# Optimization experiments

Hardware: AMD Instinct MI355X
Metric: run time of the kernel (lower is better)

## Reference

```python
import jax, jax.numpy as jnp
import numpy as np

W_DIM = 512
C_IN = 512
C_OUT = 512
K = 3
EPS = 1e-6
STYLE_SCALE = 1.0 / np.sqrt(W_DIM)              # EqualizedWeight scale for (out,in)
CONV_SCALE = 1.0 / np.sqrt(C_IN * K * K)        # EqualizedWeight scale for (out,in,k,k)


def setup_inputs() -> dict:
    key = jax.random.key(0)
    ks = jax.random.split(key, 6)
    B, H, W = 16, 64, 64
    return {
        "x": jax.random.normal(ks[0], (B, C_IN, H, W), dtype=jnp.float32),
        "w": jax.random.normal(ks[1], (B, W_DIM), dtype=jnp.float32),
        "style_weight": jax.random.normal(ks[2], (C_IN, W_DIM), dtype=jnp.float32),
        "style_bias": jnp.zeros((C_IN,), dtype=jnp.float32),
        "conv_weight": jax.random.normal(ks[3], (C_OUT, C_IN, K, K), dtype=jnp.float32),
        "noise_weight": jax.random.normal(ks[4], (1, C_OUT, 1, 1), dtype=jnp.float32),
        "bias": jnp.zeros((C_OUT,), dtype=jnp.float32),
        "noise": jax.random.normal(ks[5], (B, 1, H, W), dtype=jnp.float32),
    }


def reference(x, w, style_weight, style_bias, conv_weight, noise_weight, bias, noise):
    B, _, H, Wd = x.shape
    # to_style: equalized linear  [B, C_IN]
    s = w @ (style_weight * STYLE_SCALE).T + style_bias
    # modulate: [B, C_OUT, C_IN, K, K]
    wts = (conv_weight * CONV_SCALE)[None] * s[:, None, :, None, None]
    # demodulate
    sigma = jax.lax.rsqrt(jnp.sum(wts * wts, axis=(2, 3, 4)) + EPS)  # [B, C_OUT]
    wts = wts * sigma[:, :, None, None, None]
    # grouped conv with groups = batch
    x_r = x.reshape(1, B * C_IN, H, Wd)
    w_r = wts.reshape(B * C_OUT, C_IN, K, K)
    y = jax.lax.conv_general_dilated(
        x_r, w_r, window_strides=(1, 1), padding=[(1, 1), (1, 1)],
        dimension_numbers=("NCHW", "OIHW", "NCHW"), feature_group_count=B,
    ).reshape(B, C_OUT, H, Wd)
    # noise injection + bias + leaky relu(0.2)
    y = y + noise_weight * noise + bias[None, :, None, None]
    return jax.nn.leaky_relu(y, negative_slope=0.2)
```

## Files before the change

### kernel.cpp

```cpp
#include <hip/hip_runtime.h>


typedef __attribute__((ext_vector_type(8))) short short8;
typedef __attribute__((ext_vector_type(4))) float f32x4;

#define STYLE_SCALE 0.044194173824159216f
#define CONV_SCALE  0.014731391274719742f
#define CS2         (1.0f/4608.0f)

static __device__ __forceinline__ unsigned short f2bf(float x) {
    union { float f; unsigned int u; } a; a.f = x;
    unsigned int r = a.u + 0x7fffu + ((a.u >> 16) & 1u);
    return (unsigned short)(r >> 16);
}

static __device__ __forceinline__ void gl_lds16(const void* g, void* l) {
    __builtin_amdgcn_global_load_lds(
        (const __attribute__((address_space(1))) unsigned int*)g,
        (__attribute__((address_space(3))) unsigned int*)l, 16, 0, 0);
}

__global__ void k_style(const float* __restrict__ w, const float* __restrict__ sw,
                        const float* __restrict__ sb, float* __restrict__ s) {
    int b = blockIdx.y, j0 = blockIdx.x * 64, t = threadIdx.x;
    __shared__ float wl[512];
    __shared__ float part[256];
    wl[t] = w[b*512 + t]; wl[t+256] = w[b*512 + t + 256];
    __syncthreads();
    int jl = t & 63, seg = t >> 6;
    const float4* row = (const float4*)(sw + (size_t)(j0 + jl)*512) + seg*32;
    const float*  wv  = wl + seg*128;
    float acc = 0.f;
#pragma unroll 4
    for (int k = 0; k < 32; ++k) {
        float4 v = row[k];
        acc += v.x*wv[4*k] + v.y*wv[4*k+1] + v.z*wv[4*k+2] + v.w*wv[4*k+3];
    }
    part[t] = acc;
    __syncthreads();
    if (t < 64)
        s[b*512 + j0 + t] = (part[t] + part[t+64] + part[t+128] + part[t+192])
                            * STYLE_SCALE + sb[j0 + t];
}

__global__ void k_wprep(const float* __restrict__ cw, float* __restrict__ csq,
                        unsigned short* __restrict__ cwt) {
    int o = blockIdx.x, t = threadIdx.x;
    __shared__ float row[4608];
    const float4* src = (const float4*)(cw + (size_t)o*4608);
    for (int i = t; i < 1152; i += 256) ((float4*)row)[i] = src[i];
    __syncthreads();
#pragma unroll
    for (int it = 0; it < 2; ++it) {
        int i = t + it*256;
        float a = 0.f;
#pragma unroll
        for (int k = 0; k < 9; ++k) { float v = row[i*9 + k]; a += v*v; }
        csq[(size_t)o*512 + i] = a * CS2;
    }
    for (int p = t; p < 576; p += 256) {
        int ic = p / 36, rem = p % 36;
        int tap = rem >> 2, g = rem & 3;
        int i0 = ic*32 + g*8;
        union { unsigned short us[8]; uint4 q; } u;
#pragma unroll
        for (int j = 0; j < 8; ++j)
            u.us[j] = f2bf(row[(i0 + j)*9 + tap] * CONV_SCALE);
        size_t dst = (((size_t)(o >> 6)*16 + ic)*36 + rem)*64 + (o & 63);
        *(uint4*)(cwt + dst*8) = u.q;
    }
}

__global__ void k_sigma(const float* __restrict__ s, const float* __restrict__ csq,
                        float* __restrict__ sig) {
    int b = blockIdx.y, o0 = blockIdx.x * 64, t = threadIdx.x;
    __shared__ float s2l[512];
    __shared__ float part[256];
    float v0 = s[b*512 + t], v1 = s[b*512 + t + 256];
    s2l[t] = v0*v0; s2l[t+256] = v1*v1;
    __syncthreads();
    int ol = t & 63, seg = t >> 6;
    const float4* row = (const float4*)(csq + (size_t)(o0 + ol)*512) + seg*32;
    const float*  sv  = s2l + seg*128;
    float acc = 0.f;
#pragma unroll 4
    for (int k = 0; k < 32; ++k) {
        float4 c = row[k];
        acc += c.x*sv[4*k] + c.y*sv[4*k+1] + c.z*sv[4*k+2] + c.w*sv[4*k+3];
    }
    part[t] = acc;
    __syncthreads();
    if (t < 64)
        sig[b*512 + o0 + t] = 1.0f / sqrtf(part[t] + part[t+64] + part[t+128]
                                           + part[t+192] + 1e-6f);
}

__global__ void k_xt(const float* __restrict__ x, const float* __restrict__ s,
                     unsigned short* __restrict__ xt) {
    int h = blockIdx.x, b = blockIdx.y, t = threadIdx.x;
    __shared__ float tile[64][65];
    __shared__ float sl[64];
    for (int c0 = 0; c0 < 512; c0 += 64) {
        if (t < 64) sl[t] = s[b*512 + c0 + t];
#pragma unroll
        for (int it = 0; it < 4; ++it) {
            int idx = t + it*256;
            int c = idx >> 4, w4 = (idx & 15) * 4;
            float4 v = *(const float4*)(x + ((size_t)(b*512 + c0 + c)*4096) + h*64 + w4);
            tile[c][w4]   = v.x; tile[c][w4+1] = v.y;
            tile[c][w4+2] = v.z; tile[c][w4+3] = v.w;
        }
        __syncthreads();
#pragma unroll
        for (int it = 0; it < 2; ++it) {
            int idx = t + it*256;
            int wq = idx >> 3, c = (idx & 7) * 8;
            union { unsigned short us[8]; uint4 q; } u;
#pragma unroll
            for (int j = 0; j < 8; ++j)
                u.us[j] = f2bf(tile[c + j][wq] * sl[c + j]);
            *(uint4*)(xt + ((size_t)(b*4096 + h*64 + wq)*512 + c0 + c)) = u.q;
        }
        __syncthreads();
    }
}

__global__ __launch_bounds__(256, 2)
void k_conv(const unsigned short* __restrict__ xt, const unsigned short* __restrict__ cwt,
            const float* __restrict__ sig, const float* __restrict__ nw,
            const float* __restrict__ bias, const float* __restrict__ noise,
            float* __restrict__ out) {
    __shared__ __align__(16) short xs_s[2][20480];

    const int tid  = threadIdx.x;
    const int lane = tid & 63;
    const int wave = tid >> 6;
    const int quad = lane >> 4;
    const int l15  = lane & 15;

    const int flat  = blockIdx.x;
    const int chunk = flat & 7, idx = flat >> 3;
    const int pxblk = idx & 7;
    const int oblk  = (idx >> 3) & 7;
    const int b     = chunk*2 + (idx >> 6);
    const int o0 = oblk * 64, h0 = pxblk * 8;

    if (h0 == 0)
        for (int i = tid; i < 1024; i += 256) {
            ((unsigned int*)xs_s[0])[i] = 0u;
            ((unsigned int*)xs_s[1])[i] = 0u;
        }
    if (h0 == 56)
        for (int i = tid; i < 1024; i += 256) {
            ((unsigned int*)xs_s[0])[9*1024 + i] = 0u;
            ((unsigned int*)xs_s[1])[9*1024 + i] = 0u;
        }

    const int pp = lane >> 2;
    const int cg = (lane & 3) ^ ((lane >> 3) & 3);

#define STAGE(bufidx, icn) do {                                              \
        short* dst_ = xs_s[bufidx];                                          \
        for (int q_ = wave; q_ < 40; q_ += 4) {                              \
            int r_ = q_ >> 2, p0_ = (q_ & 3) << 4;                           \
            int gr_ = h0 - 1 + r_;                                           \
            if (gr_ >= 0 && gr_ < 64)                                        \
                gl_lds16(xt + ((size_t)(b*4096 + gr_*64 + p0_ + pp)*512      \
                               + (icn)*32 + cg*8),                           \
                         dst_ + (r_*64 + p0_)*32);                           \
        } } while (0)

    f32x4 acc[2][4][4];
#pragma unroll
    for (int rr = 0; rr < 2; ++rr)
#pragma unroll
        for (int mt = 0; mt < 4; ++mt)
#pragma unroll
            for (int nt = 0; nt < 4; ++nt) acc[rr][mt][nt] = (f32x4){0.f,0.f,0.f,0.f};

    const unsigned short* cwbase = cwt + (size_t)oblk*294912 + (size_t)quad*512
                                       + (size_t)l15*8;

    STAGE(0, 0);
    __syncthreads();

    for (int ic = 0; ic < 16; ++ic) {
        const unsigned short* cwA = cwbase + (size_t)ic*18432;
        const short8* xp = (const short8*)xs_s[ic & 1];
        const short8 z8 = {};

#define LOADA(dst, tap) do { _Pragma("unroll")                               \
        for (int mt_ = 0; mt_ < 4; ++mt_)                                    \
            dst[mt_] = *(const short8*)(cwA + (tap)*2048 + mt_*128);         \
        } while (0)

        short8 a0A[4], a0B[4];
        LOADA(a0A, 0);
        LOADA(a0B, 3);
        __builtin_amdgcn_sched_barrier(0);
        if (ic < 15) STAGE((ic + 1) & 1, ic + 1);
        __builtin_amdgcn_sched_barrier(0);

#define TAPSTEP(AF, C0, C1) do { _Pragma("unroll")                           \
        for (int mt_ = 0; mt_ < 4; ++mt_) { _Pragma("unroll")                \
            for (int nt_ = 0; nt_ < 4; ++nt_) {                              \
                acc[0][mt_][nt_] = __builtin_amdgcn_mfma_f32_16x16x32_bf16(  \
                    AF[mt_], C0[nt_], acc[0][mt_][nt_], 0, 0, 0);            \
                acc[1][mt_][nt_] = __builtin_amdgcn_mfma_f32_16x16x32_bf16(  \
                    AF[mt_], C1[nt_], acc[1][mt_][nt_], 0, 0, 0);            \
            } } } while (0)

#define LOADB(bf, d, dx, colS) do {                                          \
            const int base_ = (2*wave + (d))*256 + (colS);                   \
            if ((dx) == 0) {                                                 \
                int a0_ = (l15 == 0) ? base_ : base_ - 64;                   \
                bf[0] = xp[a0_];        bf[1] = xp[base_];                   \
                bf[2] = xp[base_ + 64]; bf[3] = xp[base_ + 128];             \
                if (l15 == 0) bf[0] = z8;                                    \
            } else if ((dx) == 1) {                                          \
                bf[0] = xp[base_ - 64]; bf[1] = xp[base_];                   \
                bf[2] = xp[base_ + 64]; bf[3] = xp[base_ + 128];             \
            } else {                                                         \
                int a3_ = (l15 == 15) ? base_ : base_ + 128;                 \
                bf[0] = xp[base_ - 64]; bf[1] = xp[base_];                   \
                bf[2] = xp[base_ + 64]; bf[3] = xp[a3_];                     \
            }                                                                \
        } while (0)

#define DXBODY(dx, AFA, AFB) do {                                            \
            const int cs_   = l15 + (dx) + 15;                               \
            const int slot_ = quad ^ ((cs_ >> 1) & 3);                       \
            const int colS_ = cs_*4 + slot_;                                 \
            short8 bA[4], bB[4];                                             \
            LOADB(bA, 0, dx, colS_);                                         \
            LOADB(bB, 1, dx, colS_);                                         \
            if ((dx) == 2 && l15 == 15) { bA[3] = z8; bB[3] = z8; }          \
            TAPSTEP(AFA, bA, bB);                                            \
            LOADA(AFA, (dx) + 6);          \
            LOADB(bA, 2, dx, colS_);                                         \
            if ((dx) == 2 && l15 == 15) bA[3] = z8;                          \
            TAPSTEP(AFB, bB, bA);                                            \
            LOADB(bB, 3, dx, colS_);                                         \
            if ((dx) == 2 && l15 == 15) bB[3] = z8;                          \
            TAPSTEP(AFA, bA, bB);                                            \
        } while (0)

        DXBODY(0, a0A, a0B);
        {
            short8 a1A[4], a1B[4];
            LOADA(a1A, 1); LOADA(a1B, 4);
            DXBODY(1, a1A, a1B);
        }
        {
            short8 a2A[4], a2B[4];
            LOADA(a2A, 2); LOADA(a2B, 5);
            DXBODY(2, a2A, a2B);
        }
#undef DXBODY
#undef LOADB
#undef TAPSTEP
#undef LOADA
        __syncthreads();
    }
#undef STAGE

    float nz[2][4];
#pragma unroll
    for (int rr = 0; rr < 2; ++rr) {
        int h = h0 + 2*wave + rr;
#pragma unroll
        for (int nt = 0; nt < 4; ++nt) nz[rr][nt] = noise[b*4096 + h*64 + nt*16 + l15];
    }
#pragma unroll
    for (int mt = 0; mt < 4; ++mt) {
#pragma unroll
        for (int r = 0; r < 4; ++r) {
            int o = o0 + mt*16 + quad*4 + r;
            float sg  = sig[b*512 + o];
            float nwv = nw[o], bv = bias[o];
#pragma unroll
            for (int rr = 0; rr < 2; ++rr) {
                int h = h0 + 2*wave + rr;
#pragma unroll
                for (int nt = 0; nt < 4; ++nt) {
                    float v = acc[rr][mt][nt][r] * sg + nwv * nz[rr][nt] + bv;
                    v = (v >= 0.f) ? v : 0.2f * v;
                    out[((size_t)(b*512 + o)*4096) + h*64 + nt*16 + l15] = v;
                }
            }
        }
    }
}

extern "C" void kernel_launch(void* const* d_in, const int* in_sizes, int n_in,
                              void* d_out, int out_size, void* d_ws, size_t ws_size,
                              hipStream_t stream) {
    const float* x     = (const float*)d_in[0];
    const float* w     = (const float*)d_in[1];
    const float* sw    = (const float*)d_in[2];
    const float* sb    = (const float*)d_in[3];
    const float* cw    = (const float*)d_in[4];
    const float* nw    = (const float*)d_in[5];
    const float* bias  = (const float*)d_in[6];
    const float* noise = (const float*)d_in[7];
    float* out = (float*)d_out;

    char* ws = (char*)d_ws;
    unsigned short* xt  = (unsigned short*)(ws + 0);
    unsigned short* cwt = (unsigned short*)(ws + 67108864);
    float* s   = (float*)(ws + 71827456);
    float* sig = (float*)(ws + 71860224);
    float* csq = (float*)(ws + 71892992);

    k_wprep<<<512, 256, 0, stream>>>(cw, csq, cwt);
    k_style<<<dim3(8, 16), 256, 0, stream>>>(w, sw, sb, s);
    k_sigma<<<dim3(8, 16), 256, 0, stream>>>(s, csq, sig);
    k_xt   <<<dim3(64, 16), 256, 0, stream>>>(x, s, xt);
    k_conv <<<dim3(1024), 256, 0, stream>>>(xt, cwt, sig, nw, bias, noise, out);
}
```

Before: 494.7 us.

## Halve conv row tile to raise occupancy, add MFMA setprio

Each conv block now computes 4 output rows instead of 8, so each wave owns one row. This halves the accumulator registers and shrinks the LDS halo buffer, allowing 3 blocks per CU and doubling the grid. MFMA bursts are wrapped in s_setprio and the A-fragment loads are restructured per dx. The cost is more redundant halo loads (6 rows staged per 4 rows computed) and twice as many weight-fragment reloads per output pixel.

```diff
diff --git a/kernel.cpp b/kernel.cpp
--- a/kernel.cpp
+++ b/kernel.cpp
@@ -125,12 +125,12 @@
     }
 }
 
-__global__ __launch_bounds__(256, 2)
+__global__ __launch_bounds__(256, 3)
 void k_conv(const unsigned short* __restrict__ xt, const unsigned short* __restrict__ cwt,
             const float* __restrict__ sig, const float* __restrict__ nw,
             const float* __restrict__ bias, const float* __restrict__ noise,
             float* __restrict__ out) {
-    __shared__ __align__(16) short xs_s[2][20480];
+    __shared__ __align__(16) short xs_s[2][6*64*32];
 
     const int tid  = threadIdx.x;
     const int lane = tid & 63;
@@ -140,20 +140,20 @@
 
     const int flat  = blockIdx.x;
     const int chunk = flat & 7, idx = flat >> 3;
-    const int pxblk = idx & 7;
-    const int oblk  = (idx >> 3) & 7;
-    const int b     = chunk*2 + (idx >> 6);
-    const int o0 = oblk * 64, h0 = pxblk * 8;
+    const int pxblk = idx & 15;
+    const int oblk  = (idx >> 4) & 7;
+    const int b     = chunk*2 + (idx >> 7);
+    const int o0 = oblk * 64, h0 = pxblk * 4;
 
     if (h0 == 0)
         for (int i = tid; i < 1024; i += 256) {
             ((unsigned int*)xs_s[0])[i] = 0u;
             ((unsigned int*)xs_s[1])[i] = 0u;
         }
-    if (h0 == 56)
+    if (h0 == 60)
         for (int i = tid; i < 1024; i += 256) {
-            ((unsigned int*)xs_s[0])[9*1024 + i] = 0u;
-            ((unsigned int*)xs_s[1])[9*1024 + i] = 0u;
+            ((unsigned int*)xs_s[0])[5*1024 + i] = 0u;
+            ((unsigned int*)xs_s[1])[5*1024 + i] = 0u;
         }
 
     const int pp = lane >> 2;
@@ -161,7 +161,7 @@
 
 #define STAGE(bufidx, icn) do {                                              \
         short* dst_ = xs_s[bufidx];                                          \
-        for (int q_ = wave; q_ < 40; q_ += 4) {                              \
+        for (int q_ = wave; q_ < 24; q_ += 4) {                              \
             int r_ = q_ >> 2, p0_ = (q_ & 3) << 4;                           \
             int gr_ = h0 - 1 + r_;                                           \
             if (gr_ >= 0 && gr_ < 64)                                        \
@@ -170,48 +170,43 @@
                          dst_ + (r_*64 + p0_)*32);                           \
         } } while (0)
 
-    f32x4 acc[2][4][4];
-#pragma unroll
-    for (int rr = 0; rr < 2; ++rr)
-#pragma unroll
-        for (int mt = 0; mt < 4; ++mt)
-#pragma unroll
-            for (int nt = 0; nt < 4; ++nt) acc[rr][mt][nt] = (f32x4){0.f,0.f,0.f,0.f};
+    f32x4 acc[4][4];
+#pragma unroll
+    for (int mt = 0; mt < 4; ++mt)
+#pragma unroll
+        for (int nt = 0; nt < 4; ++nt) acc[mt][nt] = (f32x4){0.f,0.f,0.f,0.f};
 
     const unsigned short* cwbase = cwt + (size_t)oblk*294912 + (size_t)quad*512
                                        + (size_t)l15*8;
 
     STAGE(0, 0);
     __syncthreads();
+
+    const short8 z8 = {};
 
     for (int ic = 0; ic < 16; ++ic) {
         const unsigned short* cwA = cwbase + (size_t)ic*18432;
         const short8* xp = (const short8*)xs_s[ic & 1];
-        const short8 z8 = {};
+        if (ic < 15) STAGE((ic + 1) & 1, ic + 1);
 
 #define LOADA(dst, tap) do { _Pragma("unroll")                               \
         for (int mt_ = 0; mt_ < 4; ++mt_)                                    \
             dst[mt_] = *(const short8*)(cwA + (tap)*2048 + mt_*128);         \
         } while (0)
 
-        short8 a0A[4], a0B[4];
-        LOADA(a0A, 0);
-        LOADA(a0B, 3);
-        __builtin_amdgcn_sched_barrier(0);
-        if (ic < 15) STAGE((ic + 1) & 1, ic + 1);
-        __builtin_amdgcn_sched_barrier(0);
-
-#define TAPSTEP(AF, C0, C1) do { _Pragma("unroll")                           \
+#define TAP(AF, BF) do {                                                     \
+        __builtin_amdgcn_s_setprio(1);                                       \
+        _Pragma("unroll")                                                    \
         for (int mt_ = 0; mt_ < 4; ++mt_) { _Pragma("unroll")                \
-            for (int nt_ = 0; nt_ < 4; ++nt_) {                              \
-                acc[0][mt_][nt_] = __builtin_amdgcn_mfma_f32_16x16x32_bf16(  \
-                    AF[mt_], C0[nt_], acc[0][mt_][nt_], 0, 0, 0);            \
-                acc[1][mt_][nt_] = __builtin_amdgcn_mfma_f32_16x16x32_bf16(  \
-                    AF[mt_], C1[nt_], acc[1][mt_][nt_], 0, 0, 0);            \
-            } } } while (0)
+            for (int nt_ = 0; nt_ < 4; ++nt_)                                \
+                acc[mt_][nt_] = __builtin_amdgcn_mfma_f32_16x16x32_bf16(     \
+                    AF[mt_], BF[nt_], acc[mt_][nt_], 0, 0, 0);               \
+        }                                                                    \
+        __builtin_amdgcn_s_setprio(0);                                       \
+        } while (0)
 
 #define LOADB(bf, d, dx, colS) do {                                          \
-            const int base_ = (2*wave + (d))*256 + (colS);                   \
+            const int base_ = (wave + (d))*256 + (colS);                     \
             if ((dx) == 0) {                                                 \
                 int a0_ = (l15 == 0) ? base_ : base_ - 64;                   \
                 bf[0] = xp[a0_];        bf[1] = xp[base_];                   \
@@ -227,50 +222,39 @@
             }                                                                \
         } while (0)
 
-#define DXBODY(dx, AFA, AFB) do {                                            \
+#define DXBODY(dx) do {                                                      \
             const int cs_   = l15 + (dx) + 15;                               \
             const int slot_ = quad ^ ((cs_ >> 1) & 3);                       \
             const int colS_ = cs_*4 + slot_;                                 \
-            short8 bA[4], bB[4];                                             \
-            LOADB(bA, 0, dx, colS_);                                         \
-            LOADB(bB, 1, dx, colS_);                                         \
-            if ((dx) == 2 && l15 == 15) { bA[3] = z8; bB[3] = z8; }          \
-            TAPSTEP(AFA, bA, bB);                                            \
-            LOADA(AFA, (dx) + 6);          \
-            LOADB(bA, 2, dx, colS_);                                         \
-            if ((dx) == 2 && l15 == 15) bA[3] = z8;                          \
-            TAPSTEP(AFB, bB, bA);                                            \
-            LOADB(bB, 3, dx, colS_);                                         \
-            if ((dx) == 2 && l15 == 15) bB[3] = z8;                          \
-            TAPSTEP(AFA, bA, bB);                                            \
+            short8 af[4], ag[4], b0[4], b1[4];                               \
+            LOADA(af, dx);                                 \
+            LOADA(ag, (dx) + 3);                           \
+            LOADB(b0, 0, dx, colS_);                                         \
+            LOADB(b1, 1, dx, colS_);                                         \
+            if ((dx) == 2 && l15 == 15) { b0[3] = z8; b1[3] = z8; }          \
+            TAP(af, b0);                                                     \
+            LOADA(af, (dx) + 6);                 \
+            LOADB(b0, 2, dx, colS_);            \
+            if ((dx) == 2 && l15 == 15) b0[3] = z8;                          \
+            TAP(ag, b1);                                                     \
+            TAP(af, b0);                                                     \
         } while (0)
 
-        DXBODY(0, a0A, a0B);
-        {
-            short8 a1A[4], a1B[4];
-            LOADA(a1A, 1); LOADA(a1B, 4);
-            DXBODY(1, a1A, a1B);
-        }
-        {
-            short8 a2A[4], a2B[4];
-            LOADA(a2A, 2); LOADA(a2B, 5);
-            DXBODY(2, a2A, a2B);
-        }
+        DXBODY(0);
+        DXBODY(1);
+        DXBODY(2);
 #undef DXBODY
 #undef LOADB
-#undef TAPSTEP
+#undef TAP
 #undef LOADA
         __syncthreads();
     }
 #undef STAGE
 
-    float nz[2][4];
-#pragma unroll
-    for (int rr = 0; rr < 2; ++rr) {
-        int h = h0 + 2*wave + rr;
-#pragma unroll
-        for (int nt = 0; nt < 4; ++nt) nz[rr][nt] = noise[b*4096 + h*64 + nt*16 + l15];
-    }
+    const int h = h0 + wave;
+    float nz[4];
+#pragma unroll
+    for (int nt = 0; nt < 4; ++nt) nz[nt] = noise[b*4096 + h*64 + nt*16 + l15];
 #pragma unroll
     for (int mt = 0; mt < 4; ++mt) {
 #pragma unroll
@@ -279,14 +263,10 @@
             float sg  = sig[b*512 + o];
             float nwv = nw[o], bv = bias[o];
 #pragma unroll
-            for (int rr = 0; rr < 2; ++rr) {
-                int h = h0 + 2*wave + rr;
-#pragma unroll
-                for (int nt = 0; nt < 4; ++nt) {
-                    float v = acc[rr][mt][nt][r] * sg + nwv * nz[rr][nt] + bv;
-                    v = (v >= 0.f) ? v : 0.2f * v;
-                    out[((size_t)(b*512 + o)*4096) + h*64 + nt*16 + l15] = v;
-                }
+            for (int nt = 0; nt < 4; ++nt) {
+                float v = acc[mt][nt][r] * sg + nwv * nz[nt] + bv;
+                v = (v >= 0.f) ? v : 0.2f * v;
+                out[((size_t)(b*512 + o)*4096) + h*64 + nt*16 + l15] = v;
             }
         }
     }
@@ -316,5 +296,5 @@
     k_style<<<dim3(8, 16), 256, 0, stream>>>(w, sw, sb, s);
     k_sigma<<<dim3(8, 16), 256, 0, stream>>>(s, csq, sig);
     k_xt   <<<dim3(64, 16), 256, 0, stream>>>(x, s, xt);
-    k_conv <<<dim3(1024), 256, 0, stream>>>(xt, cwt, sig, nw, bias, noise, out);
-}
+    k_conv <<<dim3(2048), 256, 0, stream>>>(xt, cwt, sig, nw, bias, noise, out);
+}
```

Measured after the change: 500.6 us. Within noise of the previous version (+1.2%).
